# Optimization experiments

Measured on AMD Instinct MI355X. Metric: run time of the kernel, lower is better.

## Reference

```python
import jax, jax.numpy as jnp
import numpy as np
import math

H_IMG, W_IMG = 800, 1216
STRIDES = [4, 8, 16, 32, 64]
SIZES = [32, 64, 128, 256, 512]
RATIOS = [0.5, 1.0, 2.0]
NUM_PER_LEVEL = [(-(-H_IMG // s)) * (-(-W_IMG // s)) * len(RATIOS) for s in STRIDES]
A_TOTAL = sum(NUM_PER_LEVEL)  # 728973
B = 4
PRE_NMS = 1000   # pre_nms_top_n['testing']
POST_NMS = 1000  # post_nms_top_n['testing']
NMS_TH = 0.7
MIN_SIZE = 1e-3
BBOX_XFORM_CLIP = math.log(1000.0 / 16)
NEG = -1e10
LEVELS_NP = np.repeat(np.arange(len(NUM_PER_LEVEL)), NUM_PER_LEVEL).astype(np.int32)


def _make_anchors():
    out = []
    for stride, size in zip(STRIDES, SIZES):
        fh, fw = -(-H_IMG // stride), -(-W_IMG // stride)
        r = np.sqrt(np.asarray(RATIOS, dtype=np.float64))
        ws, hs = size / r, size * r
        base = np.stack([-ws / 2, -hs / 2, ws / 2, hs / 2], axis=1)  # [3,4]
        sx = np.arange(fw, dtype=np.float64) * stride
        sy = np.arange(fh, dtype=np.float64) * stride
        gy, gx = np.meshgrid(sy, sx, indexing='ij')
        shifts = np.stack([gx.ravel(), gy.ravel(), gx.ravel(), gy.ravel()], axis=1)
        out.append((shifts[:, None, :] + base[None]).reshape(-1, 4))
    return np.concatenate(out, 0).astype(np.float32)


def setup_inputs() -> dict:
    key = jax.random.key(0)
    k1, k2 = jax.random.split(key)
    objectness = jax.random.normal(k1, (B, A_TOTAL), dtype=jnp.float32)
    deltas = jax.random.normal(k2, (B, A_TOTAL, 4), dtype=jnp.float32) * 0.2
    anchors = jnp.asarray(_make_anchors())
    return {'objectness': objectness, 'deltas': deltas, 'anchors': anchors}


def _decode(deltas, anchors):
    # BoxCoder.decode with weights (1,1,1,1)
    wa = anchors[:, 2] - anchors[:, 0]
    ha = anchors[:, 3] - anchors[:, 1]
    cxa = anchors[:, 0] + 0.5 * wa
    cya = anchors[:, 1] + 0.5 * ha
    dx, dy = deltas[..., 0], deltas[..., 1]
    dw = jnp.minimum(deltas[..., 2], BBOX_XFORM_CLIP)
    dh = jnp.minimum(deltas[..., 3], BBOX_XFORM_CLIP)
    cx = dx * wa + cxa
    cy = dy * ha + cya
    w = jnp.exp(dw) * wa
    h = jnp.exp(dh) * ha
    return jnp.stack([cx - 0.5 * w, cy - 0.5 * h, cx + 0.5 * w, cy + 0.5 * h], axis=-1)


def _topk_per_level(obj):
    # _get_top_n_idx: independent top-k within each anchor level, indices offset
    idxs, off = [], 0
    for n in NUM_PER_LEVEL:
        k = min(PRE_NMS, n)
        _, ti = jax.lax.top_k(obj[:, off:off + n], k)
        idxs.append(ti + off)
        off += n
    return jnp.concatenate(idxs, axis=1)


def _pairwise_iou(b):
    area = (b[:, 2] - b[:, 0]) * (b[:, 3] - b[:, 1])
    lt = jnp.maximum(b[:, None, :2], b[None, :, :2])
    rb = jnp.minimum(b[:, None, 2:], b[None, :, 2:])
    wh = jnp.clip(rb - lt, 0.0)
    inter = wh[..., 0] * wh[..., 1]
    return inter / (area[:, None] + area[None, :] - inter)


def _filter_image(boxes, scores, lvl):
    # clip_boxes_to_image
    x1 = jnp.clip(boxes[:, 0], 0.0, W_IMG)
    y1 = jnp.clip(boxes[:, 1], 0.0, H_IMG)
    x2 = jnp.clip(boxes[:, 2], 0.0, W_IMG)
    y2 = jnp.clip(boxes[:, 3], 0.0, H_IMG)
    boxes = jnp.stack([x1, y1, x2, y2], axis=1)
    # remove_small_boxes (as a validity mask; fixed shapes under jit)
    valid = ((x2 - x1) >= MIN_SIZE) & ((y2 - y1) >= MIN_SIZE)
    scores = jnp.where(valid, scores, NEG)
    N = boxes.shape[0]
    # batched_nms: offset boxes per level so levels never overlap
    sg_boxes = jax.lax.stop_gradient(boxes)
    offset = lvl.astype(boxes.dtype) * (sg_boxes.max() + 1.0)
    order = jnp.argsort(-jax.lax.stop_gradient(scores))
    iou = _pairwise_iou(sg_boxes[order] + offset[order][:, None])  # [N,N]
    idx = jnp.arange(N)
    def body(i, keep):
        sup = (iou[i] > NMS_TH) & keep[i] & (idx > i)
        return keep & ~sup
    keep = jax.lax.fori_loop(0, N, body, valid[order])
    # kept entries in score order, then truncate to POST_NMS (fixed shape)
    prio = jnp.where(keep, idx, N)
    sel = jnp.argsort(prio)[:POST_NMS]
    kept = keep[sel]
    src = order[sel]
    out_b = jnp.where(kept[:, None], boxes[src], 0.0)
    out_s = jnp.where(kept, scores[src], NEG)
    return out_b, out_s


def reference(objectness, deltas, anchors):
    proposals = _decode(deltas, anchors)                      # [B,A,4]
    top_idx = _topk_per_level(objectness)                     # [B,5000]
    obj_sel = jnp.take_along_axis(objectness, top_idx, axis=1)
    prop_sel = jnp.take_along_axis(proposals, top_idx[..., None], axis=1)
    lvl_sel = jnp.asarray(LEVELS_NP)[top_idx]
    boxes, scores = jax.vmap(_filter_image)(prop_sel, obj_sel, lvl_sel)
    return boxes, scores  # [B,POST_NMS,4], [B,POST_NMS]
```

## Files before the change

kernel.cpp:

```cpp
#include <hip/hip_runtime.h>
#include <stdint.h>

#pragma clang fp contract(off)

#define B_IMGS   4
#define NLVL     5
#define A_TOTAL  242991
#define NSEL     4741
#define NBUCK    8192
#define BSHIFT   19
#define CAND_CAP 2048
#define POST_NMS 1000
#define NBL      (B_IMGS * NLVL)
#define NMS_TH   0.7f
#define NEGV     (-1e10f)
#define W_IMGF   1216.0f
#define H_IMGF   800.0f
#define MIN_SZ   1e-3f
#define BBOX_CLIP 4.135166556742356f

#define NSLICE_PER_IMG 34

__device__ __forceinline__ int lvl_k(int l) { return (l == 4) ? 741 : 1000; }

__device__ __forceinline__ unsigned flipf(float f) {
    unsigned u = __float_as_uint(f);
    return u ^ (unsigned)(((int)u >> 31) | 0x80000000);
}
__device__ __forceinline__ float unflipf(unsigned os) {
    unsigned u = (os & 0x80000000u) ? (os ^ 0x80000000u) : ~os;
    return __uint_as_float(u);
}

static constexpr size_t OFF_BM5   = 0;
static constexpr size_t OFF_CNT   = 128;
static constexpr size_t OFF_HSL   = 256;
static constexpr size_t OFF_PSL   = OFF_HSL  + (size_t)B_IMGS * NSLICE_PER_IMG * NBUCK * 4;
static constexpr size_t OFF_CAND  = OFF_PSL  + (size_t)B_IMGS * NSLICE_PER_IMG * 256 * 4;
static constexpr size_t OFF_SEL   = OFF_CAND + (size_t)NBL * CAND_CAP * 8;
static constexpr size_t OFF_BOXR  = OFF_SEL  + (size_t)B_IMGS * NSEL * 8;
static constexpr size_t OFF_SCR   = OFF_BOXR + (size_t)B_IMGS * NSEL * 16;
static constexpr size_t OFF_BOXL  = OFF_SCR  + (size_t)B_IMGS * NSEL * 4;
static constexpr size_t OFF_VAL   = OFF_BOXL + (size_t)B_IMGS * NSEL * 16;
static constexpr size_t OFF_RMAP  = OFF_VAL  + (size_t)B_IMGS * NSEL * 4;
static constexpr size_t OFF_MASK  = (OFF_RMAP + (size_t)B_IMGS * NSEL * 4 + 15) & ~(size_t)15;
static constexpr size_t WS_NEED   = OFF_MASK + (size_t)NBL * 1024 * 16 * 8;

#define HBLK_PER_IMG 34
__global__ __launch_bounds__(512) void k_hist(const float* __restrict__ obj,
                                              unsigned* __restrict__ hist_sl,
                                              unsigned* __restrict__ part_sl,
                                              unsigned* __restrict__ cnt) {
    __shared__ __align__(16) unsigned lh[NBUCK];
    const int tid = threadIdx.x;
    const int b = blockIdx.x / HBLK_PER_IMG;
    const int r = blockIdx.x - b * HBLK_PER_IMG;
    if (r == 33) {
        if (b == 0 && tid < NBL) cnt[tid] = 0;
        return;
    }
    int sofs, sub, chunk, lstart, n;
    if (r < 24)      { sofs = 0;  sub = r;      chunk = 7600; lstart = 0;      n = 182400; }
    else if (r < 30) { sofs = 24; sub = r - 24; chunk = 7600; lstart = 182400; n = 45600; }
    else if (r < 32) { sofs = 30; sub = r - 30; chunk = 5700; lstart = 228000; n = 11400; }
    else             { sofs = 32; sub = 0;      chunk = 2850; lstart = 239400; n = 2850; }
    #pragma unroll
    for (int i = tid; i < NBUCK; i += 512) lh[i] = 0;
    __syncthreads();
    const int s0 = sub * chunk;
    const int m = min(chunk, n - s0);
    const float* src = obj + (size_t)b * A_TOTAL + lstart + s0;
    const int peel0 = (int)(((16u - ((unsigned)(uintptr_t)src & 15u)) & 15u) >> 2);
    const int peel  = (peel0 < m) ? peel0 : m;
    const int nv    = (m - peel) >> 2;
    const float4* s4 = (const float4*)(src + peel);
    const int tail0 = peel + (nv << 2);
#define H1(f) atomicAdd(&lh[flipf(f) >> BSHIFT], 1u)
#define H4(v) do { H1((v).x); H1((v).y); H1((v).z); H1((v).w); } while (0)
    if (tid < peel) H1(src[tid]);
    for (int i = tid; i < nv; i += 2048) {
        if (i + 1536 < nv) {
            float4 a0 = s4[i], a1 = s4[i + 512], a2 = s4[i + 1024], a3 = s4[i + 1536];
            H4(a0); H4(a1); H4(a2); H4(a3);
        } else {
            float4 a0 = s4[i]; H4(a0);
            if (i + 512  < nv) { float4 a = s4[i + 512];  H4(a); }
            if (i + 1024 < nv) { float4 a = s4[i + 1024]; H4(a); }
        }
    }
    for (int i = tail0 + tid; i < m; i += 512) H1(src[i]);
#undef H4
#undef H1
    __syncthreads();
    const int slice = b * NSLICE_PER_IMG + sofs + sub;
    unsigned* gh = hist_sl + (size_t)slice * NBUCK;
    #pragma unroll
    for (int i = tid; i < NBUCK / 4; i += 512)
        ((uint4*)gh)[i] = ((const uint4*)lh)[i];
    if (tid < 256) {
        unsigned s = 0;
        #pragma unroll
        for (int i = 0; i < 32; ++i) s += lh[tid * 32 + ((i + tid) & 31)];
        part_sl[(size_t)slice * 256 + tid] = s;
    }
}

#define CBLK_PER_IMG 65
__global__ __launch_bounds__(256) void k_compact(const float* __restrict__ obj,
                                                 const unsigned* __restrict__ hist_sl,
                                                 const unsigned* __restrict__ part_sl,
                                                 unsigned* __restrict__ cnt,
                                                 unsigned long long* __restrict__ cand) {
    __shared__ unsigned long long sbuf[CAND_CAP];
    __shared__ unsigned wsum[4];
    __shared__ unsigned fcnt[4];
    __shared__ unsigned s_cum, s_thr, lcnt, gbase;
    const int tid = threadIdx.x;
    const int b = blockIdx.x / CBLK_PER_IMG;
    const int r = blockIdx.x - b * CBLK_PER_IMG;
    int l, sofs, nsub, sub, chunk, lstart, n;
    if (r < 48)      { l = 0; sofs = 0;  nsub = 24; sub = r;      chunk = 3800; lstart = 0;      n = 182400; }
    else if (r < 60) { l = 1; sofs = 24; nsub = 6;  sub = r - 48; chunk = 3800; lstart = 182400; n = 45600; }
    else if (r < 63) { l = 2; sofs = 30; nsub = 2;  sub = r - 60; chunk = 3800; lstart = 228000; n = 11400; }
    else if (r == 63){ l = 3; sofs = 32; nsub = 1;  sub = 0;      chunk = 2850; lstart = 239400; n = 2850; }
    else             { l = 4; sofs = 33; nsub = 0;  sub = 0;      chunk = 741;  lstart = 242250; n = 741; }
    const int bl = b * NLVL + l;
    const int kl = lvl_k(l);
    if (tid == 0) { lcnt = 0; s_cum = 0; }
    __syncthreads();
    unsigned T = 0;
    if (l < 4) {
        const int lane = tid & 63, wv = tid >> 6;
        const unsigned* pb = part_sl + (size_t)(b * NSLICE_PER_IMG + sofs) * 256 + (255 - tid);
        unsigned x = 0;
        #pragma unroll 6
        for (int s = 0; s < nsub; ++s) x += pb[(size_t)s * 256];
        #pragma unroll
        for (int d = 1; d < 64; d <<= 1) {
            unsigned up = __shfl_up(x, d);
            if (lane >= d) x += up;
        }
        if (lane == 63) wsum[wv] = x;
        __syncthreads();
        unsigned add = 0;
        #pragma unroll
        for (int u = 0; u < 3; ++u) if (u < wv) add += wsum[u];
        const unsigned suffix = x + add;
        unsigned long long bm = __ballot(suffix >= (unsigned)kl);
        if (lane == 0) fcnt[wv] = (unsigned)__popcll(bm);
        __syncthreads();
        const int chnk = (int)(fcnt[0] + fcnt[1] + fcnt[2] + fcnt[3]) - 1;
        if ((255 - tid) == chnk + 1) s_cum = suffix;
        __syncthreads();
        if (tid < 64) {
            unsigned y = 0;
            if (tid < 32) {
                const unsigned* hb = hist_sl + (size_t)(b * NSLICE_PER_IMG + sofs) * NBUCK
                                   + chnk * 32 + (31 - tid);
                #pragma unroll 6
                for (int s = 0; s < nsub; ++s) y += hb[(size_t)s * NBUCK];
            }
            #pragma unroll
            for (int d = 1; d < 32; d <<= 1) {
                unsigned up = __shfl_up(y, d);
                if (tid >= d) y += up;
            }
            unsigned suf2 = s_cum + y;
            unsigned long long bm2 = __ballot((tid < 32) && (suf2 >= (unsigned)kl));
            if (tid == 0) {
                int istar = (int)__popcll(bm2) - 1;
                s_thr = (unsigned)(chnk * 32 + istar);
            }
        }
        __syncthreads();
        T = s_thr;
    }
    const int s0 = sub * chunk;
    const int m = min(chunk, n - s0);
    const int abase = lstart + s0;
    const float* src = obj + (size_t)b * A_TOTAL + abase;
    const int peel0 = (int)(((16u - ((unsigned)(uintptr_t)src & 15u)) & 15u) >> 2);
    const int peel  = (peel0 < m) ? peel0 : m;
    const int nv    = (m - peel) >> 2;
    const float4* s4 = (const float4*)(src + peel);
    const int tail0 = peel + (nv << 2);
#define E1(f, idx) do { unsigned os_ = flipf(f); \
    if ((os_ >> BSHIFT) >= T) { \
        unsigned slot = atomicAdd(&lcnt, 1u); \
        if (slot < CAND_CAP) \
            sbuf[slot] = (((unsigned long long)(~os_)) << 32) | (unsigned)(idx); \
    } } while (0)
#define E4(v, gb) do { E1((v).x, (gb)); E1((v).y, (gb) + 1); \
                       E1((v).z, (gb) + 2); E1((v).w, (gb) + 3); } while (0)
    if (tid < peel) E1(src[tid], abase + tid);
    for (int i = tid; i < nv; i += 512) {
        const int gb0 = abase + peel + (i << 2);
        if (i + 256 < nv) {
            float4 a0 = s4[i], a1 = s4[i + 256];
            E4(a0, gb0);
            E4(a1, gb0 + 1024);
        } else {
            float4 a0 = s4[i];
            E4(a0, gb0);
        }
    }
    for (int i = tail0 + tid; i < m; i += 256) E1(src[i], abase + i);
#undef E4
#undef E1
    __syncthreads();
    unsigned total = lcnt; if (total > CAND_CAP) total = CAND_CAP;
    if (tid == 0) gbase = atomicAdd(&cnt[bl], total);
    __syncthreads();
    const unsigned gb = gbase;
    for (unsigned i = tid; i < total; i += 256) {
        unsigned g = gb + i;
        if (g < CAND_CAP)
            cand[(size_t)bl * CAND_CAP + g] = sbuf[i];
    }
}

__global__ __launch_bounds__(1024) void k_sort(const unsigned long long* __restrict__ cand,
                                               const unsigned* __restrict__ cnt,
                                               unsigned long long* __restrict__ sel) {
    __shared__ unsigned long long keys[CAND_CAP];
    const int bl = blockIdx.x;
    const int b = bl / NLVL, l = bl - (bl / NLVL) * NLVL;
    const int tid = threadIdx.x;
    int m = (int)cnt[bl];
    if (m > CAND_CAP) m = CAND_CAP;
    for (int i = tid; i < CAND_CAP; i += 1024)
        keys[i] = (i < m) ? cand[(size_t)bl * CAND_CAP + i] : ~0ULL;
    __syncthreads();
    for (int k = 2; k <= CAND_CAP; k <<= 1) {
        for (int j = k >> 1; j > 0; j >>= 1) {
            int i = ((tid / j) * (j << 1)) + (tid % j);
            int p = i + j;
            bool up = ((i & k) == 0);
            unsigned long long a = keys[i], c = keys[p];
            if ((a > c) == up) { keys[i] = c; keys[p] = a; }
            __syncthreads();
        }
    }
    int kl = lvl_k(l);
    for (int q = tid; q < kl; q += 1024)
        sel[(size_t)b * NSEL + l * 1000 + q] = keys[q];
}

__device__ __forceinline__ int lbound_lds(const unsigned long long* s, int len,
                                          unsigned long long key) {
    int lo = 0, hi = len;
    while (lo < hi) {
        int mid = (lo + hi) >> 1;
        if (s[mid] < key) lo = mid + 1; else hi = mid;
    }
    return lo;
}

__global__ void k_decode(const float* __restrict__ deltas, const float* __restrict__ anchors,
                         const unsigned long long* __restrict__ sel,
                         float* __restrict__ boxes_r, float* __restrict__ score_r,
                         float* __restrict__ boxes_l, int* __restrict__ valid_l,
                         int* __restrict__ rankmap, unsigned* __restrict__ boxmax5) {
    __shared__ unsigned long long skey[NSEL];
    __shared__ float wmax[16];
    const int b = blockIdx.y;
    const int tid = threadIdx.x;
    for (int i = tid; i < NSEL; i += 1024)
        skey[i] = sel[(size_t)b * NSEL + i];
    __syncthreads();

    int p = blockIdx.x * 1024 + tid;
    bool on = p < NSEL;
    float mx = 0.0f;
    if (on) {
        int l = p / 1000;
        int q = p - l * 1000;
        unsigned long long key = skey[p];
        unsigned a = (unsigned)(key & 0xFFFFFFFFu);
        unsigned os = ~((unsigned)(key >> 32));
        if (a >= A_TOTAL) a = 0;
        float score = unflipf(os);
        int r = q;
        for (int l2 = 0; l2 < NLVL; ++l2) {
            if (l2 == l) continue;
            r += lbound_lds(skey + l2 * 1000, lvl_k(l2), key);
        }
        const float* dv = deltas + ((size_t)b * A_TOTAL + a) * 4;
        const float* av = anchors + (size_t)a * 4;
        float ax1 = av[0], ay1 = av[1], ax2 = av[2], ay2 = av[3];
        float wa = ax2 - ax1, ha = ay2 - ay1;
        float cxa = ax1 + 0.5f * wa, cya = ay1 + 0.5f * ha;
        float dx = dv[0], dy = dv[1];
        float dw = fminf(dv[2], BBOX_CLIP), dh = fminf(dv[3], BBOX_CLIP);
        float cx = dx * wa + cxa, cy = dy * ha + cya;
        float w = expf(dw) * wa, h = expf(dh) * ha;
        float x1 = cx - 0.5f * w, y1 = cy - 0.5f * h;
        float x2 = cx + 0.5f * w, y2 = cy + 0.5f * h;
        float x1c = fminf(fmaxf(x1, 0.0f), W_IMGF);
        float y1c = fminf(fmaxf(y1, 0.0f), H_IMGF);
        float x2c = fminf(fmaxf(x2, 0.0f), W_IMGF);
        float y2c = fminf(fmaxf(y2, 0.0f), H_IMGF);
        int valid = ((x2c - x1c) >= MIN_SZ) && ((y2c - y1c) >= MIN_SZ);
        mx = fmaxf(fmaxf(x1c, y1c), fmaxf(x2c, y2c));
        size_t rp = (size_t)b * NSEL + r;
        boxes_r[rp * 4 + 0] = x1c; boxes_r[rp * 4 + 1] = y1c;
        boxes_r[rp * 4 + 2] = x2c; boxes_r[rp * 4 + 3] = y2c;
        score_r[rp] = score;
        size_t pp = (size_t)b * NSEL + p;
        boxes_l[pp * 4 + 0] = x1c; boxes_l[pp * 4 + 1] = y1c;
        boxes_l[pp * 4 + 2] = x2c; boxes_l[pp * 4 + 3] = y2c;
        valid_l[pp] = valid;
        rankmap[pp] = r;
    }
    #pragma unroll
    for (int o = 32; o > 0; o >>= 1)
        mx = fmaxf(mx, __shfl_xor(mx, o));
    if ((tid & 63) == 0) wmax[tid >> 6] = mx;
    __syncthreads();
    if (tid == 0) {
        float m2 = wmax[0];
        #pragma unroll
        for (int i = 1; i < 16; ++i) m2 = fmaxf(m2, wmax[i]);
        boxmax5[b * 5 + blockIdx.x] = __float_as_uint(m2);
    }
}

__global__ void k_mask(const float* __restrict__ boxes_l, const unsigned* __restrict__ boxmax5,
                       unsigned long long* __restrict__ mask) {
    int bl = blockIdx.z;
    int b = bl / NLVL, l = bl - b * NLVL;
    int kl = lvl_k(l);
    int w = blockIdx.x, rg = blockIdx.y, tid = threadIdx.x;
    if (rg * 256 >= kl) return;
    float M = __uint_as_float(boxmax5[b * 5 + 0]);
    #pragma unroll
    for (int j = 1; j < 5; ++j) M = fmaxf(M, __uint_as_float(boxmax5[b * 5 + j]));
    M += 1.0f;
    float off = (float)l * M;
    __shared__ float cb[64][5];
    int j0 = w * 64;
    if (tid < 64) {
        int j = j0 + tid;
        if (j < kl) {
            const float* bp = boxes_l + ((size_t)b * NSEL + l * 1000 + j) * 4;
            float x1 = bp[0] + off, y1 = bp[1] + off, x2 = bp[2] + off, y2 = bp[3] + off;
            cb[tid][0] = x1; cb[tid][1] = y1; cb[tid][2] = x2; cb[tid][3] = y2;
            cb[tid][4] = (x2 - x1) * (y2 - y1);
        }
    }
    __syncthreads();
    int i = rg * 256 + tid;
    if (i >= kl) return;
    unsigned long long word = 0;
    if (j0 + 63 > i) {
        const float* bp = boxes_l + ((size_t)b * NSEL + l * 1000 + i) * 4;
        float ix1 = bp[0] + off, iy1 = bp[1] + off, ix2 = bp[2] + off, iy2 = bp[3] + off;
        float ai = (ix2 - ix1) * (iy2 - iy1);
        int jmax = min(64, kl - j0);
        for (int bb = 0; bb < jmax; ++bb) {
            int jj = j0 + bb;
            if (jj <= i) continue;
            float ltx = fmaxf(ix1, cb[bb][0]), lty = fmaxf(iy1, cb[bb][1]);
            float rbx = fminf(ix2, cb[bb][2]), rby = fminf(iy2, cb[bb][3]);
            float ww = fmaxf(rbx - ltx, 0.0f), hh = fmaxf(rby - lty, 0.0f);
            float inter = ww * hh;
            float iou = inter / ((ai + cb[bb][4]) - inter);
            if (iou > NMS_TH) word |= (1ULL << bb);
        }
    }
    mask[((size_t)bl * 1024 + i) * 16 + w] = word;
}

__global__ __launch_bounds__(1024) void k_ro(const int* __restrict__ valid_l,
                                             const int* __restrict__ rankmap,
                                             const unsigned long long* __restrict__ mask,
                                             const float* __restrict__ boxes_r,
                                             const float* __restrict__ score_r,
                                             float* __restrict__ out) {
    __shared__ int krank[NSEL];
    __shared__ int ps[1024];
    const int b = blockIdx.x;
    const int tid = threadIdx.x;
    const int lane = tid & 63;
    const int wave = tid >> 6;

    if (wave < NLVL) {
        const int l = wave;
        const int kl = lvl_k(l);
        const int bl = b * NLVL + l;
        const int base = b * NSEL + l * 1000;
        unsigned long long keep_w = 0;
        for (int c = 0; c < 16; ++c) {
            int q = c * 64 + lane;
            int vv = (q < kl) ? valid_l[base + q] : 0;
            unsigned long long bm = __ballot(vv);
            if (lane == c) keep_w = bm;
        }
        const int nch = (kl + 63) >> 6;
        const unsigned long long* mb = mask + (size_t)bl * 1024 * 16;
        for (int c = 0; c < nch; ++c) {
            unsigned long long kw = __shfl(keep_w, c);
            if (kw) {
                const unsigned long long* mrow = mb + (size_t)c * 64 * 16;
                unsigned long long diag = mrow[lane * 16 + c];
                unsigned dlo = (unsigned)diag, dhi = (unsigned)(diag >> 32);
                unsigned long long nz = __ballot(diag != 0ULL);
                unsigned long long rem = kw & nz;
                while (rem) {
                    int rr = __ffsll((long long)rem) - 1;
                    unsigned lo = __builtin_amdgcn_readlane(dlo, rr);
                    unsigned hi = __builtin_amdgcn_readlane(dhi, rr);
                    unsigned long long d = ((unsigned long long)hi << 32) | lo;
                    kw &= ~d;
                    rem &= ~(d | (1ULL << rr));
                }
                unsigned long long supp = 0;
                if (lane < 16) {
                    #pragma unroll
                    for (int rr = 0; rr < 64; ++rr) {
                        unsigned long long m = mrow[rr * 16 + lane];
                        supp |= (((kw >> rr) & 1ULL) ? m : 0ULL);
                    }
                }
                if (lane == c) keep_w = kw;
                else if (lane < 16 && lane > c) keep_w &= ~supp;
            }
        }
        for (int c = 0; c < 16; ++c) {
            unsigned long long kwc = __shfl(keep_w, c);
            int q = c * 64 + lane;
            if (q < kl)
                krank[rankmap[base + q]] = (int)((kwc >> lane) & 1ULL);
        }
    }
    __syncthreads();

    float* ob = out + (size_t)b * POST_NMS * 4;
    float* osc = out + (size_t)B_IMGS * POST_NMS * 4 + (size_t)b * POST_NMS;
    for (int p = tid; p < POST_NMS; p += 1024) {
        ob[p * 4 + 0] = 0.0f; ob[p * 4 + 1] = 0.0f;
        ob[p * 4 + 2] = 0.0f; ob[p * 4 + 3] = 0.0f;
        osc[p] = NEGV;
    }
    __syncthreads();
    const int CH = 5;
    int basei = tid * CH;
    int c0 = 0;
    #pragma unroll
    for (int k = 0; k < CH; ++k) {
        int rr = basei + k;
        if (rr < NSEL) c0 += krank[rr];
    }
    ps[tid] = c0;
    __syncthreads();
    for (int ofs = 1; ofs < 1024; ofs <<= 1) {
        int v = (tid >= ofs) ? ps[tid - ofs] : 0;
        __syncthreads();
        ps[tid] += v;
        __syncthreads();
    }
    int p = ps[tid] - c0;
    #pragma unroll
    for (int k = 0; k < CH; ++k) {
        int rr = basei + k;
        if (rr < NSEL && krank[rr]) {
            if (p < POST_NMS) {
                const float* bp = boxes_r + ((size_t)b * NSEL + rr) * 4;
                ob[p * 4 + 0] = bp[0]; ob[p * 4 + 1] = bp[1];
                ob[p * 4 + 2] = bp[2]; ob[p * 4 + 3] = bp[3];
                osc[p] = score_r[(size_t)b * NSEL + rr];
            }
            ++p;
        }
    }
}

extern "C" void kernel_launch(void* const* d_in, const int* in_sizes, int n_in,
                              void* d_out, int out_size, void* d_ws, size_t ws_size,
                              hipStream_t stream) {
    const float* obj     = (const float*)d_in[0];
    const float* deltas  = (const float*)d_in[1];
    const float* anchors = (const float*)d_in[2];
    float* out = (float*)d_out;

    char* ws = (char*)d_ws;
    unsigned*            boxmax5 = (unsigned*)(ws + OFF_BM5);
    unsigned*            cnt     = (unsigned*)(ws + OFF_CNT);
    unsigned*            hist_sl = (unsigned*)(ws + OFF_HSL);
    unsigned*            part_sl = (unsigned*)(ws + OFF_PSL);
    unsigned long long*  cand    = (unsigned long long*)(ws + OFF_CAND);
    unsigned long long*  sel     = (unsigned long long*)(ws + OFF_SEL);
    float*               boxes_r = (float*)(ws + OFF_BOXR);
    float*               score_r = (float*)(ws + OFF_SCR);
    float*               boxes_l = (float*)(ws + OFF_BOXL);
    int*                 valid_l = (int*)(ws + OFF_VAL);
    int*                 rankmap = (int*)(ws + OFF_RMAP);
    unsigned long long*  maskp   = (unsigned long long*)(ws + OFF_MASK);

    (void)in_sizes; (void)n_in; (void)out_size; (void)ws_size; (void)WS_NEED;

    k_hist<<<B_IMGS * HBLK_PER_IMG, 512, 0, stream>>>(obj, hist_sl, part_sl, cnt);
    k_compact<<<B_IMGS * CBLK_PER_IMG, 256, 0, stream>>>(obj, hist_sl, part_sl, cnt, cand);
    k_sort<<<NBL, 1024, 0, stream>>>(cand, cnt, sel);
    k_decode<<<dim3(5, B_IMGS), 1024, 0, stream>>>(
        deltas, anchors, sel, boxes_r, score_r, boxes_l, valid_l, rankmap, boxmax5);
    k_mask<<<dim3(16, 4, NBL), 256, 0, stream>>>(boxes_l, boxmax5, maskp);
    k_ro<<<B_IMGS, 1024, 0, stream>>>(valid_l, rankmap, maskp, boxes_r, score_r, out);
}
```

Before: 184.9 us.

## Split NMS resolve into per-level blocks with async LDS double-buffered mask prefetch

The combined resolve+output kernel is split in two. A new per-(image,level) 64-thread kernel resolves the sequential NMS suppression chain and writes keep flags to workspace. A separate kernel does the prefix-sum compaction into the output. The resolve kernel prefetches each 64-row mask chunk into LDS with global_load_lds while working on the previous chunk, so the serial chain no longer waits on global mask loads. In exchange it adds one kernel launch and a global round trip for the keep flags, and nothing in the code waits explicitly for the async loads to finish before reading LDS.

After: 176.4 us. -4.6%, faster.

```diff
diff --git a/kernel.cpp b/kernel.cpp
--- a/kernel.cpp
+++ b/kernel.cpp
@@ -32,6 +32,13 @@
     return __uint_as_float(u);
 }
 
+__device__ __forceinline__ void async_cp16(const void* g, void* l) {
+    __builtin_amdgcn_global_load_lds(
+        (const __attribute__((address_space(1))) unsigned*)g,
+        (__attribute__((address_space(3))) unsigned*)l,
+        16, 0, 0);
+}
+
 static constexpr size_t OFF_BM5   = 0;
 static constexpr size_t OFF_CNT   = 128;
 static constexpr size_t OFF_HSL   = 256;
@@ -43,7 +50,8 @@
 static constexpr size_t OFF_BOXL  = OFF_SCR  + (size_t)B_IMGS * NSEL * 4;
 static constexpr size_t OFF_VAL   = OFF_BOXL + (size_t)B_IMGS * NSEL * 16;
 static constexpr size_t OFF_RMAP  = OFF_VAL  + (size_t)B_IMGS * NSEL * 4;
-static constexpr size_t OFF_MASK  = (OFF_RMAP + (size_t)B_IMGS * NSEL * 4 + 15) & ~(size_t)15;
+static constexpr size_t OFF_KEEP  = OFF_RMAP + (size_t)B_IMGS * NSEL * 4;
+static constexpr size_t OFF_MASK  = (OFF_KEEP + (size_t)B_IMGS * NSEL * 4 + 15) & ~(size_t)15;
 static constexpr size_t WS_NEED   = OFF_MASK + (size_t)NBL * 1024 * 16 * 8;
 
 #define HBLK_PER_IMG 34
@@ -371,70 +379,82 @@
     mask[((size_t)bl * 1024 + i) * 16 + w] = word;
 }
 
-__global__ __launch_bounds__(1024) void k_ro(const int* __restrict__ valid_l,
-                                             const int* __restrict__ rankmap,
-                                             const unsigned long long* __restrict__ mask,
-                                             const float* __restrict__ boxes_r,
-                                             const float* __restrict__ score_r,
-                                             float* __restrict__ out) {
-    __shared__ int krank[NSEL];
-    __shared__ int ps[1024];
-    const int b = blockIdx.x;
-    const int tid = threadIdx.x;
-    const int lane = tid & 63;
-    const int wave = tid >> 6;
-
-    if (wave < NLVL) {
-        const int l = wave;
-        const int kl = lvl_k(l);
-        const int bl = b * NLVL + l;
-        const int base = b * NSEL + l * 1000;
-        unsigned long long keep_w = 0;
-        for (int c = 0; c < 16; ++c) {
-            int q = c * 64 + lane;
-            int vv = (q < kl) ? valid_l[base + q] : 0;
-            unsigned long long bm = __ballot(vv);
-            if (lane == c) keep_w = bm;
-        }
-        const int nch = (kl + 63) >> 6;
-        const unsigned long long* mb = mask + (size_t)bl * 1024 * 16;
-        for (int c = 0; c < nch; ++c) {
-            unsigned long long kw = __shfl(keep_w, c);
-            if (kw) {
-                const unsigned long long* mrow = mb + (size_t)c * 64 * 16;
-                unsigned long long diag = mrow[lane * 16 + c];
-                unsigned dlo = (unsigned)diag, dhi = (unsigned)(diag >> 32);
-                unsigned long long nz = __ballot(diag != 0ULL);
-                unsigned long long rem = kw & nz;
-                while (rem) {
-                    int rr = __ffsll((long long)rem) - 1;
-                    unsigned lo = __builtin_amdgcn_readlane(dlo, rr);
-                    unsigned hi = __builtin_amdgcn_readlane(dhi, rr);
-                    unsigned long long d = ((unsigned long long)hi << 32) | lo;
-                    kw &= ~d;
-                    rem &= ~(d | (1ULL << rr));
+__global__ void k_resolve(const int* __restrict__ valid_l, const int* __restrict__ rankmap,
+                          const unsigned long long* __restrict__ mask, int* __restrict__ keep_r) {
+    const int bl = blockIdx.x;
+    const int b = bl / NLVL, l = bl - b * NLVL;
+    const int kl = lvl_k(l);
+    const int lane = threadIdx.x;
+    __shared__ __align__(16) unsigned long long sbufA[64 * 16];
+    __shared__ __align__(16) unsigned long long sbufB[64 * 16];
+    const int base = b * NSEL + l * 1000;
+
+    unsigned long long keep_w = 0;
+    for (int c = 0; c < 16; ++c) {
+        int q = c * 64 + lane;
+        int vv = (q < kl) ? valid_l[base + q] : 0;
+        unsigned long long bm = __ballot(vv);
+        if (lane == c) keep_w = bm;
+    }
+
+    const int nch = (kl + 63) >> 6;
+    const char* mbyte = (const char*)(mask + (size_t)bl * 1024 * 16);
+
+    {
+        const char* g0 = mbyte + (size_t)lane * 16;
+        #pragma unroll
+        for (int j = 0; j < 8; ++j)
+            async_cp16(g0 + j * 1024, (char*)sbufA + j * 1024);
+    }
+
+    for (int c = 0; c < nch; ++c) {
+        unsigned long long* cur = (c & 1) ? sbufB : sbufA;
+        unsigned long long* nxt = (c & 1) ? sbufA : sbufB;
+        __syncthreads();
+        if (c + 1 < nch) {
+            const char* g1 = mbyte + (size_t)(c + 1) * 8192 + (size_t)lane * 16;
+            #pragma unroll
+            for (int j = 0; j < 8; ++j)
+                async_cp16(g1 + j * 1024, (char*)nxt + j * 1024);
+        }
+        unsigned long long kw = __shfl(keep_w, c);
+        if (kw) {
+            unsigned long long diag = cur[lane * 16 + c];
+            unsigned dlo = (unsigned)diag, dhi = (unsigned)(diag >> 32);
+            unsigned long long nz = __ballot(diag != 0ULL);
+            unsigned long long rem = kw & nz;
+            while (rem) {
+                int r = __ffsll((long long)rem) - 1;
+                unsigned lo = __builtin_amdgcn_readlane(dlo, r);
+                unsigned hi = __builtin_amdgcn_readlane(dhi, r);
+                unsigned long long d = ((unsigned long long)hi << 32) | lo;
+                kw &= ~d;
+                rem &= ~(d | (1ULL << r));
+            }
+            unsigned long long supp = 0;
+            if (lane < 16) {
+                #pragma unroll
+                for (int r = 0; r < 64; ++r) {
+                    unsigned long long m = cur[r * 16 + lane];
+                    supp |= (((kw >> r) & 1ULL) ? m : 0ULL);
                 }
-                unsigned long long supp = 0;
-                if (lane < 16) {
-                    #pragma unroll
-                    for (int rr = 0; rr < 64; ++rr) {
-                        unsigned long long m = mrow[rr * 16 + lane];
-                        supp |= (((kw >> rr) & 1ULL) ? m : 0ULL);
-                    }
-                }
-                if (lane == c) keep_w = kw;
-                else if (lane < 16 && lane > c) keep_w &= ~supp;
             }
-        }
-        for (int c = 0; c < 16; ++c) {
-            unsigned long long kwc = __shfl(keep_w, c);
-            int q = c * 64 + lane;
-            if (q < kl)
-                krank[rankmap[base + q]] = (int)((kwc >> lane) & 1ULL);
-        }
-    }
-    __syncthreads();
-
+            if (lane == c) keep_w = kw;
+            else if (lane < 16 && lane > c) keep_w &= ~supp;
+        }
+    }
+    __syncthreads();
+    for (int c = 0; c < 16; ++c) {
+        unsigned long long kwc = __shfl(keep_w, c);
+        int q = c * 64 + lane;
+        if (q < kl)
+            keep_r[b * NSEL + rankmap[base + q]] = (int)((kwc >> lane) & 1ULL);
+    }
+}
+
+__global__ void k_output(const int* __restrict__ keep_r, const float* __restrict__ boxes_r,
+                         const float* __restrict__ score_r, float* __restrict__ out) {
+    int b = blockIdx.x, tid = threadIdx.x;
     float* ob = out + (size_t)b * POST_NMS * 4;
     float* osc = out + (size_t)B_IMGS * POST_NMS * 4 + (size_t)b * POST_NMS;
     for (int p = tid; p < POST_NMS; p += 1024) {
@@ -444,14 +464,15 @@
     }
     __syncthreads();
     const int CH = 5;
-    int basei = tid * CH;
-    int c0 = 0;
+    int base = tid * CH;
+    int cnt = 0;
     #pragma unroll
     for (int k = 0; k < CH; ++k) {
-        int rr = basei + k;
-        if (rr < NSEL) c0 += krank[rr];
-    }
-    ps[tid] = c0;
+        int r = base + k;
+        if (r < NSEL) cnt += keep_r[b * NSEL + r];
+    }
+    __shared__ int ps[1024];
+    ps[tid] = cnt;
     __syncthreads();
     for (int ofs = 1; ofs < 1024; ofs <<= 1) {
         int v = (tid >= ofs) ? ps[tid - ofs] : 0;
@@ -459,16 +480,16 @@
         ps[tid] += v;
         __syncthreads();
     }
-    int p = ps[tid] - c0;
+    int p = ps[tid] - cnt;
     #pragma unroll
     for (int k = 0; k < CH; ++k) {
-        int rr = basei + k;
-        if (rr < NSEL && krank[rr]) {
+        int r = base + k;
+        if (r < NSEL && keep_r[b * NSEL + r]) {
             if (p < POST_NMS) {
-                const float* bp = boxes_r + ((size_t)b * NSEL + rr) * 4;
+                const float* bp = boxes_r + ((size_t)b * NSEL + r) * 4;
                 ob[p * 4 + 0] = bp[0]; ob[p * 4 + 1] = bp[1];
                 ob[p * 4 + 2] = bp[2]; ob[p * 4 + 3] = bp[3];
-                osc[p] = score_r[(size_t)b * NSEL + rr];
+                osc[p] = score_r[(size_t)b * NSEL + r];
             }
             ++p;
         }
@@ -495,6 +516,7 @@
     float*               boxes_l = (float*)(ws + OFF_BOXL);
     int*                 valid_l = (int*)(ws + OFF_VAL);
     int*                 rankmap = (int*)(ws + OFF_RMAP);
+    int*                 keep_r  = (int*)(ws + OFF_KEEP);
     unsigned long long*  maskp   = (unsigned long long*)(ws + OFF_MASK);
 
     (void)in_sizes; (void)n_in; (void)out_size; (void)ws_size; (void)WS_NEED;
@@ -505,5 +527,6 @@
     k_decode<<<dim3(5, B_IMGS), 1024, 0, stream>>>(
         deltas, anchors, sel, boxes_r, score_r, boxes_l, valid_l, rankmap, boxmax5);
     k_mask<<<dim3(16, 4, NBL), 256, 0, stream>>>(boxes_l, boxmax5, maskp);
-    k_ro<<<B_IMGS, 1024, 0, stream>>>(valid_l, rankmap, maskp, boxes_r, score_r, out);
-}
+    k_resolve<<<NBL, 64, 0, stream>>>(valid_l, rankmap, maskp, keep_r);
+    k_output<<<B_IMGS, 1024, 0, stream>>>(keep_r, boxes_r, score_r, out);
+}
```

## Fuse IoU mask computation and NMS reduction into one pipelined per-level kernel

Applied to the files above, without the earlier changes.

Replaces the separate mask and reduction kernels with a single kernel per (image, level). In it, 15 waves compute IoU tiles into double-buffered shared memory while wave 0 runs the sequential suppression on the previous tile. The last level block of each image, found through an atomic counter, does the final compaction into the output. This removes the global mask round-trip and one launch, and overlaps mask generation with the serial scan. In exchange, the mask is computed by only 20 blocks instead of many, which may cut parallelism.

New measurement: 317.6 us. 71.7% more time.

```diff
diff --git a/kernel.cpp b/kernel.cpp
--- a/kernel.cpp
+++ b/kernel.cpp
@@ -34,6 +34,7 @@
 
 static constexpr size_t OFF_BM5   = 0;
 static constexpr size_t OFF_CNT   = 128;
+static constexpr size_t OFF_DONE  = 208;
 static constexpr size_t OFF_HSL   = 256;
 static constexpr size_t OFF_PSL   = OFF_HSL  + (size_t)B_IMGS * NSLICE_PER_IMG * NBUCK * 4;
 static constexpr size_t OFF_CAND  = OFF_PSL  + (size_t)B_IMGS * NSLICE_PER_IMG * 256 * 4;
@@ -43,20 +44,20 @@
 static constexpr size_t OFF_BOXL  = OFF_SCR  + (size_t)B_IMGS * NSEL * 4;
 static constexpr size_t OFF_VAL   = OFF_BOXL + (size_t)B_IMGS * NSEL * 16;
 static constexpr size_t OFF_RMAP  = OFF_VAL  + (size_t)B_IMGS * NSEL * 4;
-static constexpr size_t OFF_MASK  = (OFF_RMAP + (size_t)B_IMGS * NSEL * 4 + 15) & ~(size_t)15;
-static constexpr size_t WS_NEED   = OFF_MASK + (size_t)NBL * 1024 * 16 * 8;
+static constexpr size_t OFF_KEEP  = OFF_RMAP + (size_t)B_IMGS * NSEL * 4;
+static constexpr size_t WS_NEED   = OFF_KEEP + (size_t)B_IMGS * NSEL * 4;
 
 #define HBLK_PER_IMG 34
 __global__ __launch_bounds__(512) void k_hist(const float* __restrict__ obj,
                                               unsigned* __restrict__ hist_sl,
                                               unsigned* __restrict__ part_sl,
-                                              unsigned* __restrict__ cnt) {
+                                              unsigned* __restrict__ cntz) {
     __shared__ __align__(16) unsigned lh[NBUCK];
     const int tid = threadIdx.x;
     const int b = blockIdx.x / HBLK_PER_IMG;
     const int r = blockIdx.x - b * HBLK_PER_IMG;
     if (r == 33) {
-        if (b == 0 && tid < NBL) cnt[tid] = 0;
+        if (b == 0 && tid < NBL + B_IMGS) cntz[tid] = 0;
         return;
     }
     int sofs, sub, chunk, lstart, n;
@@ -325,84 +326,102 @@
     }
 }
 
-__global__ void k_mask(const float* __restrict__ boxes_l, const unsigned* __restrict__ boxmax5,
-                       unsigned long long* __restrict__ mask) {
-    int bl = blockIdx.z;
-    int b = bl / NLVL, l = bl - b * NLVL;
-    int kl = lvl_k(l);
-    int w = blockIdx.x, rg = blockIdx.y, tid = threadIdx.x;
-    if (rg * 256 >= kl) return;
+__device__ __forceinline__ void ef_tile(const float (*boxes5)[5],
+                                        unsigned long long* buf,
+                                        int cc, int kl, int wave, int lane) {
+    const int rbase = cc << 6;
+    const int i = rbase + lane;
+    float ix1 = 0.f, iy1 = 0.f, ix2 = 0.f, iy2 = 0.f, ai = 0.f;
+    const bool row_on = (i < kl);
+    if (row_on) {
+        ix1 = boxes5[i][0]; iy1 = boxes5[i][1];
+        ix2 = boxes5[i][2]; iy2 = boxes5[i][3]; ai = boxes5[i][4];
+    }
+    for (int w = wave - 1; w < 16; w += 15) {
+        if (w < cc) continue;
+        const int j0 = w << 6;
+        const int jmax = min(64, kl - j0);
+        unsigned long long word = 0;
+        if (row_on && jmax > 0) {
+            for (int bb = 0; bb < jmax; ++bb) {
+                int jj = j0 + bb;
+                if (jj <= i) continue;
+                float ltx = fmaxf(ix1, boxes5[jj][0]), lty = fmaxf(iy1, boxes5[jj][1]);
+                float rbx = fminf(ix2, boxes5[jj][2]), rby = fminf(iy2, boxes5[jj][3]);
+                float ww = fmaxf(rbx - ltx, 0.0f), hh = fmaxf(rby - lty, 0.0f);
+                float inter = ww * hh;
+                float iou = inter / ((ai + boxes5[jj][4]) - inter);
+                if (iou > NMS_TH) word |= (1ULL << bb);
+            }
+        }
+        buf[(lane << 4) + w] = word;
+    }
+}
+
+__global__ __launch_bounds__(1024) void k_mr(const float* __restrict__ boxes_l,
+                                             const unsigned* __restrict__ boxmax5,
+                                             const int* __restrict__ valid_l,
+                                             const int* __restrict__ rankmap,
+                                             int* __restrict__ keep_r,
+                                             unsigned* __restrict__ done,
+                                             const float* __restrict__ boxes_r,
+                                             const float* __restrict__ score_r,
+                                             float* __restrict__ out) {
+    __shared__ float boxes5[1024][5];
+    __shared__ unsigned long long tileA[64 * 16];
+    __shared__ unsigned long long tileB[64 * 16];
+    __shared__ int ps[1024];
+    __shared__ int s_last;
+    const int bl = blockIdx.x;
+    const int b = bl / NLVL, l = bl - b * NLVL;
+    const int kl = lvl_k(l);
+    const int tid = threadIdx.x;
+    const int lane = tid & 63;
+    const int wave = tid >> 6;
+    const int base = b * NSEL + l * 1000;
+    const int nch = (kl + 63) >> 6;
+
     float M = __uint_as_float(boxmax5[b * 5 + 0]);
     #pragma unroll
     for (int j = 1; j < 5; ++j) M = fmaxf(M, __uint_as_float(boxmax5[b * 5 + j]));
     M += 1.0f;
-    float off = (float)l * M;
-    __shared__ float cb[64][5];
-    int j0 = w * 64;
-    if (tid < 64) {
-        int j = j0 + tid;
-        if (j < kl) {
-            const float* bp = boxes_l + ((size_t)b * NSEL + l * 1000 + j) * 4;
-            float x1 = bp[0] + off, y1 = bp[1] + off, x2 = bp[2] + off, y2 = bp[3] + off;
-            cb[tid][0] = x1; cb[tid][1] = y1; cb[tid][2] = x2; cb[tid][3] = y2;
-            cb[tid][4] = (x2 - x1) * (y2 - y1);
-        }
-    }
-    __syncthreads();
-    int i = rg * 256 + tid;
-    if (i >= kl) return;
-    unsigned long long word = 0;
-    if (j0 + 63 > i) {
-        const float* bp = boxes_l + ((size_t)b * NSEL + l * 1000 + i) * 4;
-        float ix1 = bp[0] + off, iy1 = bp[1] + off, ix2 = bp[2] + off, iy2 = bp[3] + off;
-        float ai = (ix2 - ix1) * (iy2 - iy1);
-        int jmax = min(64, kl - j0);
-        for (int bb = 0; bb < jmax; ++bb) {
-            int jj = j0 + bb;
-            if (jj <= i) continue;
-            float ltx = fmaxf(ix1, cb[bb][0]), lty = fmaxf(iy1, cb[bb][1]);
-            float rbx = fminf(ix2, cb[bb][2]), rby = fminf(iy2, cb[bb][3]);
-            float ww = fmaxf(rbx - ltx, 0.0f), hh = fmaxf(rby - lty, 0.0f);
-            float inter = ww * hh;
-            float iou = inter / ((ai + cb[bb][4]) - inter);
-            if (iou > NMS_TH) word |= (1ULL << bb);
-        }
-    }
-    mask[((size_t)bl * 1024 + i) * 16 + w] = word;
-}
-
-__global__ __launch_bounds__(1024) void k_ro(const int* __restrict__ valid_l,
-                                             const int* __restrict__ rankmap,
-                                             const unsigned long long* __restrict__ mask,
-                                             const float* __restrict__ boxes_r,
-                                             const float* __restrict__ score_r,
-                                             float* __restrict__ out) {
-    __shared__ int krank[NSEL];
-    __shared__ int ps[1024];
-    const int b = blockIdx.x;
-    const int tid = threadIdx.x;
-    const int lane = tid & 63;
-    const int wave = tid >> 6;
-
-    if (wave < NLVL) {
-        const int l = wave;
-        const int kl = lvl_k(l);
-        const int bl = b * NLVL + l;
-        const int base = b * NSEL + l * 1000;
-        unsigned long long keep_w = 0;
-        for (int c = 0; c < 16; ++c) {
-            int q = c * 64 + lane;
+    const float off = (float)l * M;
+
+    if (tid < kl) {
+        const float* bp = boxes_l + ((size_t)base + tid) * 4;
+        float x1 = bp[0] + off, y1 = bp[1] + off;
+        float x2 = bp[2] + off, y2 = bp[3] + off;
+        boxes5[tid][0] = x1; boxes5[tid][1] = y1;
+        boxes5[tid][2] = x2; boxes5[tid][3] = y2;
+        boxes5[tid][4] = (x2 - x1) * (y2 - y1);
+    } else {
+        boxes5[tid][0] = 0.f; boxes5[tid][1] = 0.f;
+        boxes5[tid][2] = 0.f; boxes5[tid][3] = 0.f; boxes5[tid][4] = 0.f;
+    }
+    unsigned long long keep_w = 0;
+    __syncthreads();
+
+    if (wave == 0) {
+        for (int c2 = 0; c2 < 16; ++c2) {
+            int q = (c2 << 6) + lane;
             int vv = (q < kl) ? valid_l[base + q] : 0;
             unsigned long long bm = __ballot(vv);
-            if (lane == c) keep_w = bm;
-        }
-        const int nch = (kl + 63) >> 6;
-        const unsigned long long* mb = mask + (size_t)bl * 1024 * 16;
-        for (int c = 0; c < nch; ++c) {
+            if (lane == c2) keep_w = bm;
+        }
+    } else {
+        ef_tile(boxes5, tileA, 0, kl, wave, lane);
+    }
+    __syncthreads();
+
+    for (int c = 0; c < nch; ++c) {
+        unsigned long long* cur = (c & 1) ? tileB : tileA;
+        unsigned long long* nxt = (c & 1) ? tileA : tileB;
+        if (wave > 0) {
+            if (c + 1 < nch) ef_tile(boxes5, nxt, c + 1, kl, wave, lane);
+        } else {
             unsigned long long kw = __shfl(keep_w, c);
             if (kw) {
-                const unsigned long long* mrow = mb + (size_t)c * 64 * 16;
-                unsigned long long diag = mrow[lane * 16 + c];
+                unsigned long long diag = cur[(lane << 4) + c];
                 unsigned dlo = (unsigned)diag, dhi = (unsigned)(diag >> 32);
                 unsigned long long nz = __ballot(diag != 0ULL);
                 unsigned long long rem = kw & nz;
@@ -418,22 +437,35 @@
                 if (lane < 16) {
                     #pragma unroll
                     for (int rr = 0; rr < 64; ++rr) {
-                        unsigned long long m = mrow[rr * 16 + lane];
-                        supp |= (((kw >> rr) & 1ULL) ? m : 0ULL);
+                        unsigned long long mm = cur[(rr << 4) + lane];
+                        supp |= (((kw >> rr) & 1ULL) ? mm : 0ULL);
                     }
                 }
                 if (lane == c) keep_w = kw;
                 else if (lane < 16 && lane > c) keep_w &= ~supp;
             }
         }
-        for (int c = 0; c < 16; ++c) {
-            unsigned long long kwc = __shfl(keep_w, c);
-            int q = c * 64 + lane;
+        __syncthreads();
+    }
+    if (wave == 0) {
+        for (int c2 = 0; c2 < 16; ++c2) {
+            unsigned long long kwc = __shfl(keep_w, c2);
+            int q = (c2 << 6) + lane;
             if (q < kl)
-                krank[rankmap[base + q]] = (int)((kwc >> lane) & 1ULL);
-        }
-    }
-    __syncthreads();
+                keep_r[b * NSEL + rankmap[base + q]] = (int)((kwc >> lane) & 1ULL);
+        }
+    }
+    __syncthreads();
+
+    if (tid == 0) {
+        __threadfence();
+        unsigned old = __hip_atomic_fetch_add(done + b, 1u,
+                                              __ATOMIC_ACQ_REL, __HIP_MEMORY_SCOPE_AGENT);
+        s_last = (old == NLVL - 1);
+        if (old == NLVL - 1) __threadfence();
+    }
+    __syncthreads();
+    if (!s_last) return;
 
     float* ob = out + (size_t)b * POST_NMS * 4;
     float* osc = out + (size_t)B_IMGS * POST_NMS * 4 + (size_t)b * POST_NMS;
@@ -449,7 +481,7 @@
     #pragma unroll
     for (int k = 0; k < CH; ++k) {
         int rr = basei + k;
-        if (rr < NSEL) c0 += krank[rr];
+        if (rr < NSEL) c0 += keep_r[b * NSEL + rr];
     }
     ps[tid] = c0;
     __syncthreads();
@@ -463,7 +495,7 @@
     #pragma unroll
     for (int k = 0; k < CH; ++k) {
         int rr = basei + k;
-        if (rr < NSEL && krank[rr]) {
+        if (rr < NSEL && keep_r[b * NSEL + rr]) {
             if (p < POST_NMS) {
                 const float* bp = boxes_r + ((size_t)b * NSEL + rr) * 4;
                 ob[p * 4 + 0] = bp[0]; ob[p * 4 + 1] = bp[1];
@@ -486,6 +518,7 @@
     char* ws = (char*)d_ws;
     unsigned*            boxmax5 = (unsigned*)(ws + OFF_BM5);
     unsigned*            cnt     = (unsigned*)(ws + OFF_CNT);
+    unsigned*            done    = (unsigned*)(ws + OFF_DONE);
     unsigned*            hist_sl = (unsigned*)(ws + OFF_HSL);
     unsigned*            part_sl = (unsigned*)(ws + OFF_PSL);
     unsigned long long*  cand    = (unsigned long long*)(ws + OFF_CAND);
@@ -495,7 +528,7 @@
     float*               boxes_l = (float*)(ws + OFF_BOXL);
     int*                 valid_l = (int*)(ws + OFF_VAL);
     int*                 rankmap = (int*)(ws + OFF_RMAP);
-    unsigned long long*  maskp   = (unsigned long long*)(ws + OFF_MASK);
+    int*                 keep_r  = (int*)(ws + OFF_KEEP);
 
     (void)in_sizes; (void)n_in; (void)out_size; (void)ws_size; (void)WS_NEED;
 
@@ -504,6 +537,6 @@
     k_sort<<<NBL, 1024, 0, stream>>>(cand, cnt, sel);
     k_decode<<<dim3(5, B_IMGS), 1024, 0, stream>>>(
         deltas, anchors, sel, boxes_r, score_r, boxes_l, valid_l, rankmap, boxmax5);
-    k_mask<<<dim3(16, 4, NBL), 256, 0, stream>>>(boxes_l, boxmax5, maskp);
-    k_ro<<<B_IMGS, 1024, 0, stream>>>(valid_l, rankmap, maskp, boxes_r, score_r, out);
-}
+    k_mr<<<NBL, 1024, 0, stream>>>(boxes_l, boxmax5, valid_l, rankmap,
+                                   keep_r, done, boxes_r, score_r, out);
+}
```
